# Kernel optimization log

Hardware: AMD Instinct MI355X
Metric: run time of the kernel (lower is better)

## Reference

```python
import jax, jax.numpy as jnp
import numpy as np

PAST = 15        # sum(num_classes[:-1])
NC = 20          # sum(num_classes)
ALPHA = 0.99
IGNORE = 255


def setup_inputs() -> dict:
    key = jax.random.key(0)
    k1, k2, k3, k4, k5, k6 = jax.random.split(key, 6)
    B, C, H, W = 8, NC, 512, 512
    logit = jax.random.normal(k1, (B, C, H, W), dtype=jnp.float32)
    # ema_prob is used as probabilities (gathered & compared to thresholds)
    ema_prob = jax.nn.softmax(jax.random.normal(k2, (B, C, H, W), dtype=jnp.float32), axis=1)
    ema_thresh = jax.random.uniform(k3, (NC,), dtype=jnp.float32, minval=0.2, maxval=0.8)
    real_labels = jax.random.randint(k4, (B, H, W), 0, NC, dtype=jnp.int64)
    # sprinkle ignore pixels (255) like real segmentation masks
    real_labels = jnp.where(jax.random.uniform(k5, (B, H, W)) < 0.1, IGNORE, real_labels)
    moving_prob_avg = jax.random.uniform(k6, (NC,), dtype=jnp.float32)
    return {"logit": logit, "ema_prob": ema_prob, "ema_thresh": ema_thresh,
            "real_labels": real_labels, "moving_prob_avg": moving_prob_avg}


def reference(logit, ema_prob, ema_thresh, real_labels, moving_prob_avg):
    # --- pseudo-labels from current model (detached softmax) ---
    logit_prob = jax.nn.softmax(jax.lax.stop_gradient(logit), axis=1)  # [B,C,H,W]
    labels = jnp.argmax(logit_prob[:, :PAST], axis=1)                   # [B,H,W]
    labels = jnp.where(real_labels >= PAST, real_labels, labels)
    idx = jnp.where(real_labels == IGNORE, 0, labels)
    scores = jnp.take_along_axis(logit_prob, idx[:, None], axis=1)[:, 0]  # [B,H,W]

    # --- per-class mean of scores + EMA update of moving_prob_avg ---
    flat_lab = labels.reshape(-1)
    flat_sc = scores.reshape(-1)
    seg = jnp.where(flat_lab == IGNORE, NC, flat_lab)  # route ignored to extra bucket
    sums = jax.ops.segment_sum(flat_sc, seg, num_segments=NC + 1)[:NC]
    counts = jax.ops.segment_sum(jnp.ones_like(flat_sc), seg, num_segments=NC + 1)[:NC]
    means = sums / jnp.maximum(counts, 1.0)
    mpa = moving_prob_avg  # numpy buffer in torch (no grad)
    new_mpa = jnp.where(counts > 0,
                        jnp.where(mpa == -1.0, means, (1.0 - ALPHA) * means + ALPHA * mpa),
                        mpa)

    # --- EMA-teacher pseudo labels + threshold mask ---
    ema_labels = jnp.argmax(ema_prob[:, :PAST], axis=1)
    ema_labels = jnp.where(real_labels >= PAST, real_labels, ema_labels)
    eidx = jnp.where(real_labels == IGNORE, 0, ema_labels)
    ema_scores = jnp.take_along_axis(ema_prob, eidx[:, None], axis=1)[:, 0]
    valid_cls = ema_labels < NC  # 255 never matches any class in the torch loop
    thr = ema_thresh[jnp.clip(ema_labels, 0, NC - 1)]
    ema_mask = valid_cls & (ema_scores >= thr)
    dynamic_labels = jnp.where(ema_mask, ema_labels, IGNORE)  # [B,H,W]

    # --- masked cross-entropy with per-class reweighting ---
    logp = jax.nn.log_softmax(logit, axis=1)
    cidx = jnp.clip(dynamic_labels, 0, NC - 1)
    losses = -jnp.take_along_axis(logp, cidx[:, None], axis=1)[:, 0]
    valid = dynamic_labels != IGNORE
    mult = jnp.where(valid, 1.0 - new_mpa[cidx], 1.0)
    losses = losses * jax.lax.stop_gradient(mult)  # multiplier is a host scalar in torch
    vs = valid.astype(losses.dtype)
    return jnp.sum(losses * vs) / jnp.sum(vs)
```

## Files before the change

kernel.cpp:

```cpp
#include <hip/hip_runtime.h>
#include <math.h>


#define PASTC 15
#define NCC   20
#define IGN   255
#define HW2   262144
#define ALPHAF 0.99f
#define NPF   6

__global__ __launch_bounds__(256) void dl_main(
    const float* __restrict__ logit,
    const float* __restrict__ ema,
    const float* __restrict__ thresh,
    const int*   __restrict__ real,
    float*       __restrict__ ws)
{
    __shared__ float s_acc[61];
    __shared__ float s_thr[NCC];
    const int tid = threadIdx.x;
    if (tid < 61) s_acc[tid] = 0.0f;
    if (tid < NCC) s_thr[tid] = thresh[tid];
    __syncthreads();

    const int t  = blockIdx.x * 256 + tid;
    const int p0 = t << 2;
    const int b  = p0 >> 18;
    const int s  = p0 & (HW2 - 1);
    const size_t base = (((size_t)(b * NCC)) << 18) + (size_t)s;
    const float* eb = ema   + base;
    const float* lb = logit + base;

    const int4 rl4 = *reinterpret_cast<const int4*>(real + p0);
    const int rl[4] = {rl4.x, rl4.y, rl4.z, rl4.w};

    int cap_ch[4];
    float e_m15[4], e_cap[4];
    float x_m15[4], x_cap[4];
    float x_earg[4];
    float se[4];
    int   e_arg[4], arg15[4];
#pragma unroll
    for (int j = 0; j < 4; ++j) {
        cap_ch[j] = (rl[j] == IGN) ? 0 : (rl[j] >= PASTC ? rl[j] : -1);
        e_m15[j] = -INFINITY; x_m15[j] = -INFINITY;
        e_cap[j] = 0.0f; x_cap[j] = 0.0f; x_earg[j] = 0.0f;
        se[j] = 0.0f; e_arg[j] = 0; arg15[j] = 0;
    }

    float4 be[NPF], bl[NPF];
#pragma unroll
    for (int c = 0; c < NPF; ++c) {
        be[c] = *reinterpret_cast<const float4*>(eb + ((size_t)c << 18));
        bl[c] = *reinterpret_cast<const float4*>(lb + ((size_t)c << 18));
    }

#pragma unroll
    for (int c = 0; c < NCC; ++c) {
        const int slot = c % NPF;
        const float4 ve = be[slot];
        const float4 vl = bl[slot];
        if (c + NPF < NCC) {
            be[slot] = *reinterpret_cast<const float4*>(eb + ((size_t)(c + NPF) << 18));
            bl[slot] = *reinterpret_cast<const float4*>(lb + ((size_t)(c + NPF) << 18));
        }
        const float ev[4] = {ve.x, ve.y, ve.z, ve.w};
        const float xv[4] = {vl.x, vl.y, vl.z, vl.w};
#pragma unroll
        for (int j = 0; j < 4; ++j) {
            const float x  = xv[j];
            se[j] += __expf(x);
            if (c < PASTC) {
                const bool gl = x > x_m15[j];
                x_m15[j] = gl ? x : x_m15[j];
                arg15[j] = gl ? c : arg15[j];
                const bool ge = ev[j] > e_m15[j];
                e_m15[j]  = ge ? ev[j] : e_m15[j];
                e_arg[j]  = ge ? c : e_arg[j];
                x_earg[j] = ge ? x : x_earg[j];
            }
            if (c == cap_ch[j]) { e_cap[j] = ev[j]; x_cap[j] = x; }
        }
    }

    float vcnt = 0.0f;
#pragma unroll
    for (int j = 0; j < 4; ++j) {
        const float lse = __logf(se[j]);
        if (rl[j] != IGN) {
            const int   lab  = (rl[j] >= PASTC) ? rl[j] : arg15[j];
            const float xsc  = (cap_ch[j] >= 0) ? x_cap[j] : x_m15[j];
            const float prob = __expf(xsc - lse);
            atomicAdd(&s_acc[lab], prob);
            atomicAdd(&s_acc[20 + lab], 1.0f);
        }
        const int   el  = (rl[j] >= PASTC) ? rl[j] : e_arg[j];
        const float esc = (rl[j] >= PASTC) ? e_cap[j] : e_m15[j];
        const float th  = s_thr[el < NCC ? el : (NCC - 1)];
        const bool  valid = (el < NCC) && (esc >= th);
        if (valid) {
            const float xel = (rl[j] >= PASTC) ? x_cap[j] : x_earg[j];
            atomicAdd(&s_acc[40 + el], lse - xel);
        }
        const unsigned long long bm = __ballot(valid);
        if ((tid & 63) == 0) vcnt += (float)__popcll(bm);
    }
    if ((tid & 63) == 0) atomicAdd(&s_acc[60], vcnt);

    __syncthreads();
    if (tid < 61) atomicAdd(&ws[tid], s_acc[tid]);
}

__global__ void dl_final(const float* __restrict__ ws,
                         const float* __restrict__ mpa,
                         float*       __restrict__ out)
{
    if (threadIdx.x == 0 && blockIdx.x == 0) {
        float acc = 0.0f;
        for (int c = 0; c < NCC; ++c) {
            const float ssum = ws[c];
            const float cnt  = ws[20 + c];
            const float lsum = ws[40 + c];
            const float m    = mpa[c];
            const float mean = ssum / fmaxf(cnt, 1.0f);
            const float nm   = (cnt > 0.0f)
                                 ? ((m == -1.0f) ? mean
                                                 : (1.0f - ALPHAF) * mean + ALPHAF * m)
                                 : m;
            acc += lsum * (1.0f - nm);
        }
        out[0] = acc / ws[60];
    }
}

extern "C" void kernel_launch(void* const* d_in, const int* in_sizes, int n_in,
                              void* d_out, int out_size, void* d_ws, size_t ws_size,
                              hipStream_t stream) {
    const float* logit  = (const float*)d_in[0];
    const float* ema    = (const float*)d_in[1];
    const float* thresh = (const float*)d_in[2];
    const int*   real   = (const int*)d_in[3];
    const float* mpa    = (const float*)d_in[4];
    float* out = (float*)d_out;
    float* ws  = (float*)d_ws;

    hipMemsetAsync(ws, 0, 64 * sizeof(float), stream);

    dl_main<<<2048, 256, 0, stream>>>(logit, ema, thresh, real, ws);
    dl_final<<<1, 64, 0, stream>>>(ws, mpa, out);
}
```

Measured before the change: 346.4 us.

## Stream channel loads directly into LDS via global_load_lds with explicit waitcnt pipeline

Result: slower. 364.5 us (+5.2%).

```diff
diff --git a/kernel.cpp b/kernel.cpp
--- a/kernel.cpp
+++ b/kernel.cpp
@@ -7,7 +7,14 @@
 #define IGN   255
 #define HW2   262144
 #define ALPHAF 0.99f
-#define NPF   6
+#define DPF   4
+
+__device__ __forceinline__ void gld_lds16(const float* g, void* l) {
+    __builtin_amdgcn_global_load_lds(
+        (const __attribute__((address_space(1))) void*)g,
+        (__attribute__((address_space(3))) void*)l,
+        16, 0, 0);
+}
 
 __global__ __launch_bounds__(256) void dl_main(
     const float* __restrict__ logit,
@@ -16,8 +23,11 @@
     const int*   __restrict__ real,
     float*       __restrict__ ws)
 {
-    __shared__ float s_acc[61];
-    __shared__ float s_thr[NCC];
+    __shared__ float4 s_e[DPF][256];
+    __shared__ float4 s_l[DPF][256];
+    __shared__ float  s_acc[61];
+    __shared__ float  s_thr[NCC];
+
     const int tid = threadIdx.x;
     if (tid < 61) s_acc[tid] = 0.0f;
     if (tid < NCC) s_thr[tid] = thresh[tid];
@@ -30,56 +40,58 @@
     const size_t base = (((size_t)(b * NCC)) << 18) + (size_t)s;
     const float* eb = ema   + base;
     const float* lb = logit + base;
+    const int wbase = tid & ~63;
 
     const int4 rl4 = *reinterpret_cast<const int4*>(real + p0);
     const int rl[4] = {rl4.x, rl4.y, rl4.z, rl4.w};
 
-    int cap_ch[4];
-    float e_m15[4], e_cap[4];
-    float x_m15[4], x_cap[4];
-    float x_earg[4];
-    float se[4];
-    int   e_arg[4], arg15[4];
+    int   cap_ch[4];
+    float se[4], x_m15[4], esel[4], xsel[4];
+    int   arg15[4], earg[4];
 #pragma unroll
     for (int j = 0; j < 4; ++j) {
         cap_ch[j] = (rl[j] == IGN) ? 0 : (rl[j] >= PASTC ? rl[j] : -1);
-        e_m15[j] = -INFINITY; x_m15[j] = -INFINITY;
-        e_cap[j] = 0.0f; x_cap[j] = 0.0f; x_earg[j] = 0.0f;
-        se[j] = 0.0f; e_arg[j] = 0; arg15[j] = 0;
+        se[j] = 0.0f; x_m15[j] = -INFINITY; esel[j] = -INFINITY;
+        xsel[j] = 0.0f; arg15[j] = 0; earg[j] = 0;
     }
 
-    float4 be[NPF], bl[NPF];
 #pragma unroll
-    for (int c = 0; c < NPF; ++c) {
-        be[c] = *reinterpret_cast<const float4*>(eb + ((size_t)c << 18));
-        bl[c] = *reinterpret_cast<const float4*>(lb + ((size_t)c << 18));
+    for (int c = 0; c < DPF; ++c) {
+        gld_lds16(eb + ((size_t)c << 18), &s_e[c][wbase]);
+        gld_lds16(lb + ((size_t)c << 18), &s_l[c][wbase]);
     }
 
 #pragma unroll
     for (int c = 0; c < NCC; ++c) {
-        const int slot = c % NPF;
-        const float4 ve = be[slot];
-        const float4 vl = bl[slot];
-        if (c + NPF < NCC) {
-            be[slot] = *reinterpret_cast<const float4*>(eb + ((size_t)(c + NPF) << 18));
-            bl[slot] = *reinterpret_cast<const float4*>(lb + ((size_t)(c + NPF) << 18));
-        }
-        const float ev[4] = {ve.x, ve.y, ve.z, ve.w};
-        const float xv[4] = {vl.x, vl.y, vl.z, vl.w};
+        const int slot = c & (DPF - 1);
+        const int vm = (c + DPF < NCC) ? 2 * (DPF - 1) : 2 * (NCC - 1 - c);
+        asm volatile("s_waitcnt vmcnt(%0)" :: "n"(vm) : "memory");
+        __builtin_amdgcn_sched_barrier(0);
+
+        const float4 ve4 = s_e[slot][tid];
+        const float4 vl4 = s_l[slot][tid];
+        const float ev[4] = {ve4.x, ve4.y, ve4.z, ve4.w};
+        const float xv[4] = {vl4.x, vl4.y, vl4.z, vl4.w};
 #pragma unroll
         for (int j = 0; j < 4; ++j) {
-            const float x  = xv[j];
+            const float x = xv[j];
             se[j] += __expf(x);
             if (c < PASTC) {
                 const bool gl = x > x_m15[j];
                 x_m15[j] = gl ? x : x_m15[j];
                 arg15[j] = gl ? c : arg15[j];
-                const bool ge = ev[j] > e_m15[j];
-                e_m15[j]  = ge ? ev[j] : e_m15[j];
-                e_arg[j]  = ge ? c : e_arg[j];
-                x_earg[j] = ge ? x : x_earg[j];
             }
-            if (c == cap_ch[j]) { e_cap[j] = ev[j]; x_cap[j] = x; }
+            const bool upd = (cap_ch[j] < 0)
+                               ? (c < PASTC && ev[j] > esel[j])
+                               : (c == cap_ch[j]);
+            esel[j] = upd ? ev[j] : esel[j];
+            earg[j] = upd ? c    : earg[j];
+            xsel[j] = upd ? x    : xsel[j];
+        }
+
+        if (c + DPF < NCC) {
+            gld_lds16(eb + ((size_t)(c + DPF) << 18), &s_e[slot][wbase]);
+            gld_lds16(lb + ((size_t)(c + DPF) << 18), &s_l[slot][wbase]);
         }
     }
 
@@ -89,18 +101,16 @@
         const float lse = __logf(se[j]);
         if (rl[j] != IGN) {
             const int   lab  = (rl[j] >= PASTC) ? rl[j] : arg15[j];
-            const float xsc  = (cap_ch[j] >= 0) ? x_cap[j] : x_m15[j];
-            const float prob = __expf(xsc - lse);
+            const float sval = (rl[j] >= PASTC) ? xsel[j] : x_m15[j];
+            const float prob = __expf(sval - lse);
             atomicAdd(&s_acc[lab], prob);
             atomicAdd(&s_acc[20 + lab], 1.0f);
         }
-        const int   el  = (rl[j] >= PASTC) ? rl[j] : e_arg[j];
-        const float esc = (rl[j] >= PASTC) ? e_cap[j] : e_m15[j];
-        const float th  = s_thr[el < NCC ? el : (NCC - 1)];
-        const bool  valid = (el < NCC) && (esc >= th);
+        const int  el    = (rl[j] >= PASTC) ? rl[j] : earg[j];
+        const float th   = s_thr[el < NCC ? el : (NCC - 1)];
+        const bool valid = (el < NCC) && (esel[j] >= th);
         if (valid) {
-            const float xel = (rl[j] >= PASTC) ? x_cap[j] : x_earg[j];
-            atomicAdd(&s_acc[40 + el], lse - xel);
+            atomicAdd(&s_acc[40 + el], lse - xsel[j]);
         }
         const unsigned long long bm = __ballot(valid);
         if ((tid & 63) == 0) vcnt += (float)__popcll(bm);
```
